# Kernel optimization log

Measured on AMD Instinct MI355X. Metric: run time of the kernel, lower is better.

The kernel has to match this reference:

```python
import jax, jax.numpy as jnp
import numpy as np

HIDDEN = 1024
FEAT = 2048
BOTTLENECK = 512
B, T = 64, 512


def setup_inputs() -> dict:
    key = jax.random.key(0)
    k1, k2, k3, k4, k5 = jax.random.split(key, 5)
    hidden = jax.random.normal(k1, (B, HIDDEN), dtype=jnp.float32)
    feats = jax.random.normal(k2, (B, T, FEAT), dtype=jnp.float32)
    # nn.Linear weights stored as [out, in]; apply as x @ W.T
    W = jax.random.normal(k3, (BOTTLENECK, HIDDEN), dtype=jnp.float32) * (1.0 / np.sqrt(HIDDEN))
    U = jax.random.normal(k4, (BOTTLENECK, FEAT), dtype=jnp.float32) * (1.0 / np.sqrt(FEAT))
    b = jnp.ones((BOTTLENECK,), dtype=jnp.float32)
    w = jax.random.normal(k5, (1, BOTTLENECK), dtype=jnp.float32) * (1.0 / np.sqrt(BOTTLENECK))
    return {"hidden": hidden, "feats": feats, "W": W, "U": U, "b": b, "w": w}


def reference(hidden, feats, W, U, b, w):
    Wh = hidden @ W.T                      # [B, K]
    Uv = jnp.einsum('btf,kf->btk', feats, U)  # [B, T, K]
    e = jnp.tanh(Wh[:, None, :] + Uv + b)  # [B, T, K]
    energies = jnp.einsum('btk,ok->bto', e, w)  # [B, T, 1]
    weights = jax.nn.softmax(energies, axis=1)  # softmax over time
    attn_feats = jnp.sum(feats * weights, axis=1)  # [B, F]
    return attn_feats, weights
```

## Files before the change

### kernel.cpp

```cpp
#include <hip/hip_runtime.h>
#include <math.h>

#define BATCH 64
#define TDIM 512
#define FEAT 2048
#define HID 1024
#define KDIM 512
#define MROWS (BATCH * TDIM)
#define TCH 16
#define TCLEN (TDIM / TCH)

#define NSTEP (FEAT / 64)
#define BSLOT (KDIM * 8)
#define BTILE (BSLOT * 8)

typedef __attribute__((ext_vector_type(8))) short short8;
typedef __attribute__((ext_vector_type(4))) float floatx4;

#define GLL16(g, l)                                                     \
    __builtin_amdgcn_global_load_lds(                                   \
        (const __attribute__((address_space(1))) void*)(g),             \
        (__attribute__((address_space(3))) void*)(l), 16, 0, 0)

__device__ __forceinline__ unsigned short f2bf(float x) {
    unsigned int u = __float_as_uint(x);
    u += 0x7FFFu + ((u >> 16) & 1u);
    return (unsigned short)(u >> 16);
}

__global__ __launch_bounds__(256) void k0n(const float* __restrict__ U,
                                           const float* __restrict__ hidden,
                                           const float* __restrict__ W,
                                           const float* __restrict__ bias,
                                           unsigned short* __restrict__ uBt,
                                           float* __restrict__ whb) {
    int bx = blockIdx.x;
    if (bx < 256) {
        const int NS = NSTEP * BSLOT;
        for (int s = bx * 256 + threadIdx.x; s < NS; s += 256 * 256) {
            int t   = s >> 12;
            int rem = s & 4095;
            int r   = rem >> 3;
            int c   = (rem & 7) ^ (r & 7);
            const float* src = U + (size_t)r * FEAT + t * 64 + c * 8;
            float4 v0 = *(const float4*)src;
            float4 v1 = *(const float4*)(src + 4);
            ushort4 o0, o1;
            o0.x = f2bf(v0.x); o0.y = f2bf(v0.y); o0.z = f2bf(v0.z); o0.w = f2bf(v0.w);
            o1.x = f2bf(v1.x); o1.y = f2bf(v1.y); o1.z = f2bf(v1.z); o1.w = f2bf(v1.w);
            ((ushort4*)uBt)[s * 2]     = o0;
            ((ushort4*)uBt)[s * 2 + 1] = o1;
        }
    } else {
        int bid = bx - 256;
        int b = bid >> 7;
        int k = (bid & 127) * 4 + (threadIdx.x >> 6);
        int lane = threadIdx.x & 63;
        const float* hrow = hidden + (size_t)b * HID;
        const float* wrow = W + (size_t)k * HID;
        float acc = 0.f;
        #pragma unroll 4
        for (int h = lane; h < HID; h += 64) acc += hrow[h] * wrow[h];
        #pragma unroll
        for (int off = 32; off > 0; off >>= 1) acc += __shfl_down(acc, off, 64);
        if (lane == 0) whb[b * KDIM + k] = acc + bias[k];
    }
}

__global__ __launch_bounds__(512, 2) void k2n(const float* __restrict__ feats,
                                              const unsigned short* __restrict__ uBt,
                                              const float* __restrict__ whb,
                                              const float* __restrict__ wvec,
                                              float* __restrict__ energies) {
    __shared__ __align__(16) unsigned short As[128 * 64];
    __shared__ __align__(16) unsigned short Bs[2][512 * 64];
    __shared__ float sums[4][128];

    const int tid  = threadIdx.x;
    const int wave = tid >> 6;
    const int lane = tid & 63;
    const int row0 = blockIdx.x * 128;
    const int wm = wave >> 2;
    const int wn = wave & 3;
    const int col = lane & 15, quad = lane >> 4;

    const int sr = tid >> 3;
    const int sc = (tid & 7) ^ (sr & 7);
    const float* gA = feats + (size_t)(row0 + sr) * FEAT + sc * 8;
    unsigned short* lA0 = As + tid * 8;
    unsigned short* lA1 = As + (tid + 512) * 8;

    const unsigned short* gB = uBt + (size_t)(wave * 512 + lane) * 8;

    floatx4 acc[4][8];
    #pragma unroll
    for (int i = 0; i < 4; ++i)
        #pragma unroll
        for (int j = 0; j < 8; ++j) acc[i][j] = (floatx4){0.f, 0.f, 0.f, 0.f};

    float4 a0 = *(const float4*)(gA);
    float4 a1 = *(const float4*)(gA + 4);
    float4 a2 = *(const float4*)(gA + (size_t)64 * FEAT);
    float4 a3 = *(const float4*)(gA + (size_t)64 * FEAT + 4);
    gA += 64;
    #pragma unroll
    for (int g = 0; g < 8; ++g)
        GLL16(gB + g * 512, &Bs[0][(wave * 512 + g * 64) * 8]);
    {
        short8 w0, w1;
        w0[0] = f2bf(a0.x); w0[1] = f2bf(a0.y); w0[2] = f2bf(a0.z); w0[3] = f2bf(a0.w);
        w0[4] = f2bf(a1.x); w0[5] = f2bf(a1.y); w0[6] = f2bf(a1.z); w0[7] = f2bf(a1.w);
        w1[0] = f2bf(a2.x); w1[1] = f2bf(a2.y); w1[2] = f2bf(a2.z); w1[3] = f2bf(a2.w);
        w1[4] = f2bf(a3.x); w1[5] = f2bf(a3.y); w1[6] = f2bf(a3.z); w1[7] = f2bf(a3.w);
        *(short8*)lA0 = w0;
        *(short8*)lA1 = w1;
    }
    __syncthreads();

    int nb = 0;
    for (int t = 0; t < NSTEP; ++t) {
        if (t < NSTEP - 1) {
            a0 = *(const float4*)(gA);
            a1 = *(const float4*)(gA + 4);
            a2 = *(const float4*)(gA + (size_t)64 * FEAT);
            a3 = *(const float4*)(gA + (size_t)64 * FEAT + 4);
            gA += 64;
            const unsigned short* gb = gB + (size_t)(t + 1) * BTILE;
            unsigned short* lb = &Bs[nb ^ 1][(wave * 512) * 8];
            #pragma unroll
            for (int g = 0; g < 8; ++g)
                GLL16(gb + g * 512, lb + g * 512);
        }

        #pragma unroll
        for (int kk = 0; kk < 2; ++kk) {
            const int sw = ((kk * 4 + quad) ^ (col & 7)) * 8;
            short8 af[4], bf[8];
            #pragma unroll
            for (int i = 0; i < 4; ++i)
                af[i] = *(const short8*)&As[(wm * 64 + i * 16 + col) * 64 + sw];
            #pragma unroll
            for (int j = 0; j < 8; ++j)
                bf[j] = *(const short8*)&Bs[nb][(wn * 128 + j * 16 + col) * 64 + sw];
            #pragma unroll
            for (int i = 0; i < 4; ++i)
                #pragma unroll
                for (int j = 0; j < 8; ++j)
                    acc[i][j] = __builtin_amdgcn_mfma_f32_16x16x32_bf16(
                        af[i], bf[j], acc[i][j], 0, 0, 0);
        }
        __syncthreads();

        if (t < NSTEP - 1) {
            short8 w0, w1;
            w0[0] = f2bf(a0.x); w0[1] = f2bf(a0.y); w0[2] = f2bf(a0.z); w0[3] = f2bf(a0.w);
            w0[4] = f2bf(a1.x); w0[5] = f2bf(a1.y); w0[6] = f2bf(a1.z); w0[7] = f2bf(a1.w);
            w1[0] = f2bf(a2.x); w1[1] = f2bf(a2.y); w1[2] = f2bf(a2.z); w1[3] = f2bf(a2.w);
            w1[4] = f2bf(a3.x); w1[5] = f2bf(a3.y); w1[6] = f2bf(a3.z); w1[7] = f2bf(a3.w);
            *(short8*)lA0 = w0;
            *(short8*)lA1 = w1;
            __syncthreads();
        }
        nb ^= 1;
    }

    const int b = row0 >> 9;
    float wk[8], hk[8];
    #pragma unroll
    for (int j = 0; j < 8; ++j) {
        int k = wn * 128 + j * 16 + col;
        wk[j] = wvec[k];
        hk[j] = whb[b * KDIM + k];
    }
    #pragma unroll
    for (int i = 0; i < 4; ++i) {
        #pragma unroll
        for (int r = 0; r < 4; ++r) {
            float s = 0.f;
            #pragma unroll
            for (int j = 0; j < 8; ++j)
                s += tanhf(acc[i][j][r] + hk[j]) * wk[j];
            #pragma unroll
            for (int off = 8; off > 0; off >>= 1)
                s += __shfl_down(s, off, 16);
            if (col == 0)
                sums[wn][wm * 64 + i * 16 + quad * 4 + r] = s;
        }
    }
    __syncthreads();
    if (tid < 128)
        energies[row0 + tid] =
            sums[0][tid] + sums[1][tid] + sums[2][tid] + sums[3][tid];
}

__global__ __launch_bounds__(512) void k3n(const float* __restrict__ energies,
                                           float* __restrict__ wout) {
    int b = blockIdx.x;
    int t = threadIdx.x;
    float e = energies[b * TDIM + t];

    __shared__ float sm[512];
    sm[t] = e;
    __syncthreads();
    #pragma unroll
    for (int s = 256; s > 0; s >>= 1) {
        if (t < s) sm[t] = fmaxf(sm[t], sm[t + s]);
        __syncthreads();
    }
    float m = sm[0];
    __syncthreads();
    float ex = __expf(e - m);
    sm[t] = ex;
    __syncthreads();
    #pragma unroll
    for (int s = 256; s > 0; s >>= 1) {
        if (t < s) sm[t] += sm[t + s];
        __syncthreads();
    }
    float inv = 1.f / sm[0];
    wout[b * TDIM + t] = ex * inv;
}

__global__ __launch_bounds__(256) void k4n(const float* __restrict__ feats,
                                           const float* __restrict__ weights,
                                           float* __restrict__ partial4) {
    int b  = blockIdx.y;
    int t0 = blockIdx.x * TCLEN;
    int f8 = threadIdx.x * 8;
    __shared__ float wsm[TCLEN];
    if (threadIdx.x < TCLEN) wsm[threadIdx.x] = weights[b * TDIM + t0 + threadIdx.x];
    __syncthreads();

    const float* fp = feats + ((size_t)b * TDIM + t0) * FEAT + f8;
    float a[8];
    #pragma unroll
    for (int e = 0; e < 8; ++e) a[e] = 0.f;
    #pragma unroll 4
    for (int t = 0; t < TCLEN; ++t) {
        float4 v0 = *(const float4*)(fp + (size_t)t * FEAT);
        float4 v1 = *(const float4*)(fp + (size_t)t * FEAT + 4);
        float w = wsm[t];
        a[0] += v0.x * w; a[1] += v0.y * w; a[2] += v0.z * w; a[3] += v0.w * w;
        a[4] += v1.x * w; a[5] += v1.y * w; a[6] += v1.z * w; a[7] += v1.w * w;
    }
    float* op = partial4 + ((size_t)blockIdx.x * BATCH + b) * FEAT + f8;
    float4 o0 = {a[0], a[1], a[2], a[3]};
    float4 o1 = {a[4], a[5], a[6], a[7]};
    *(float4*)op = o0;
    *(float4*)(op + 4) = o1;
}

__global__ __launch_bounds__(256) void k5_reduce(const float* __restrict__ partial4,
                                                 float* __restrict__ out) {
    int i4 = blockIdx.x * 256 + threadIdx.x;
    float4 s = ((const float4*)partial4)[i4];
    #pragma unroll
    for (int c = 1; c < TCH; ++c) {
        float4 v = ((const float4*)partial4)[(size_t)c * (BATCH * FEAT / 4) + i4];
        s.x += v.x; s.y += v.y; s.z += v.z; s.w += v.w;
    }
    ((float4*)out)[i4] = s;
}

#define BM 128
#define BN 128
#define BF 16
#define LDSPAD 4

__global__ __launch_bounds__(256) void k1_whb(const float* __restrict__ hidden,
                                              const float* __restrict__ W,
                                              const float* __restrict__ bias,
                                              float* __restrict__ whb) {
    int b = blockIdx.y;
    int k = blockIdx.x * 4 + (threadIdx.x >> 6);
    int lane = threadIdx.x & 63;
    const float* hrow = hidden + (size_t)b * HID;
    const float* wrow = W + (size_t)k * HID;
    float acc = 0.f;
    #pragma unroll 4
    for (int h = lane; h < HID; h += 64) acc += hrow[h] * wrow[h];
    #pragma unroll
    for (int off = 32; off > 0; off >>= 1) acc += __shfl_down(acc, off, 64);
    if (lane == 0) whb[b * KDIM + k] = acc + bias[k];
}

__global__ __launch_bounds__(256) void k2_energy(const float* __restrict__ feats,
                                                 const float* __restrict__ U,
                                                 const float* __restrict__ whb,
                                                 const float* __restrict__ wvec,
                                                 float* __restrict__ partial) {
    __shared__ __align__(16) float As[BF][BM + LDSPAD];
    __shared__ __align__(16) float Us[BF][BN + LDSPAD];

    const int row0 = blockIdx.x * BM;
    const int k0   = blockIdx.y * BN;
    const int tid  = threadIdx.x;
    const int tx   = tid & 15;
    const int ty   = tid >> 4;

    float acc[8][8];
    #pragma unroll
    for (int i = 0; i < 8; ++i)
        #pragma unroll
        for (int j = 0; j < 8; ++j) acc[i][j] = 0.f;

    for (int f0 = 0; f0 < FEAT; f0 += BF) {
        #pragma unroll
        for (int l = 0; l < 2; ++l) {
            int li = tid + l * 256;
            int r  = li >> 2;
            int c4 = (li & 3) * 4;
            float4 av = *(const float4*)(feats + (size_t)(row0 + r) * FEAT + f0 + c4);
            float4 uv = *(const float4*)(U     + (size_t)(k0   + r) * FEAT + f0 + c4);
            As[c4 + 0][r] = av.x; As[c4 + 1][r] = av.y;
            As[c4 + 2][r] = av.z; As[c4 + 3][r] = av.w;
            Us[c4 + 0][r] = uv.x; Us[c4 + 1][r] = uv.y;
            Us[c4 + 2][r] = uv.z; Us[c4 + 3][r] = uv.w;
        }
        __syncthreads();
        #pragma unroll
        for (int kf = 0; kf < BF; ++kf) {
            float4 a0 = *(const float4*)&As[kf][ty * 8];
            float4 a1 = *(const float4*)&As[kf][ty * 8 + 4];
            float4 u0 = *(const float4*)&Us[kf][tx * 8];
            float4 u1 = *(const float4*)&Us[kf][tx * 8 + 4];
            float a[8] = {a0.x, a0.y, a0.z, a0.w, a1.x, a1.y, a1.z, a1.w};
            float u[8] = {u0.x, u0.y, u0.z, u0.w, u1.x, u1.y, u1.z, u1.w};
            #pragma unroll
            for (int i = 0; i < 8; ++i)
                #pragma unroll
                for (int j = 0; j < 8; ++j) acc[i][j] += a[i] * u[j];
        }
        __syncthreads();
    }

    const int b = row0 >> 9;
    float psum[8];
    #pragma unroll
    for (int i = 0; i < 8; ++i) {
        float s = 0.f;
        #pragma unroll
        for (int j = 0; j < 8; ++j) {
            int k = k0 + tx * 8 + j;
            s += tanhf(acc[i][j] + whb[b * KDIM + k]) * wvec[k];
        }
        psum[i] = s;
    }
    #pragma unroll
    for (int off = 8; off > 0; off >>= 1)
        #pragma unroll
        for (int i = 0; i < 8; ++i) psum[i] += __shfl_down(psum[i], off, 16);

    if (tx == 0) {
        int c = blockIdx.y;
        #pragma unroll
        for (int i = 0; i < 8; ++i)
            partial[c * MROWS + row0 + ty * 8 + i] = psum[i];
    }
}

__global__ __launch_bounds__(512) void k3_softmax(const float* __restrict__ partial,
                                                  float* __restrict__ wout) {
    int b = blockIdx.x;
    int t = threadIdx.x;
    float e = 0.f;
    #pragma unroll
    for (int c = 0; c < 4; ++c) e += partial[c * MROWS + b * TDIM + t];

    __shared__ float sm[512];
    sm[t] = e;
    __syncthreads();
    #pragma unroll
    for (int s = 256; s > 0; s >>= 1) {
        if (t < s) sm[t] = fmaxf(sm[t], sm[t + s]);
        __syncthreads();
    }
    float m = sm[0];
    __syncthreads();
    float ex = __expf(e - m);
    sm[t] = ex;
    __syncthreads();
    #pragma unroll
    for (int s = 256; s > 0; s >>= 1) {
        if (t < s) sm[t] += sm[t + s];
        __syncthreads();
    }
    float inv = 1.f / sm[0];
    wout[b * TDIM + t] = ex * inv;
}

__global__ __launch_bounds__(256) void k4_direct(const float* __restrict__ feats,
                                                 const float* __restrict__ weights,
                                                 float* __restrict__ out) {
    int b = blockIdx.y;
    int f4 = (blockIdx.x * 256 + threadIdx.x) * 4;
    __shared__ float wsm[TDIM];
    wsm[threadIdx.x]       = weights[b * TDIM + threadIdx.x];
    wsm[threadIdx.x + 256] = weights[b * TDIM + 256 + threadIdx.x];
    __syncthreads();

    const float* fp = feats + (size_t)b * TDIM * FEAT + f4;
    float ax = 0.f, ay = 0.f, az = 0.f, aw = 0.f;
    for (int t = 0; t < TDIM; ++t) {
        float4 v = *(const float4*)(fp + (size_t)t * FEAT);
        float w = wsm[t];
        ax += v.x * w; ay += v.y * w; az += v.z * w; aw += v.w * w;
    }
    float4 o = {ax, ay, az, aw};
    *(float4*)(out + (size_t)b * FEAT + f4) = o;
}

extern "C" void kernel_launch(void* const* d_in, const int* in_sizes, int n_in,
                              void* d_out, int out_size, void* d_ws, size_t ws_size,
                              hipStream_t stream) {
    const float* hidden = (const float*)d_in[0];
    const float* feats  = (const float*)d_in[1];
    const float* W      = (const float*)d_in[2];
    const float* U      = (const float*)d_in[3];
    const float* bias   = (const float*)d_in[4];
    const float* wvec   = (const float*)d_in[5];

    float* out         = (float*)d_out;
    float* attn_out    = out;
    float* weights_out = out + (size_t)BATCH * FEAT;
    float* whb         = weights_out;
    float* energies    = attn_out;

    const size_t uN        = (size_t)KDIM * FEAT;
    const size_t uBytes    = uN * sizeof(unsigned short);
    const size_t poolBytes = (size_t)TCH * BATCH * FEAT * sizeof(float);
    const bool fast = ws_size >= uBytes + poolBytes;

    if (fast) {
        unsigned short* uBt = (unsigned short*)d_ws;
        float* pool4 = (float*)((char*)d_ws + uBytes);
        k0n<<<dim3(256 + 8192), 256, 0, stream>>>(U, hidden, W, bias, uBt, whb);
        k2n<<<dim3(MROWS / 128), 512, 0, stream>>>(feats, uBt, whb, wvec, energies);
        k3n<<<dim3(BATCH), 512, 0, stream>>>(energies, weights_out);
        k4n<<<dim3(TCH, BATCH), 256, 0, stream>>>(feats, weights_out, pool4);
        k5_reduce<<<dim3(BATCH * FEAT / 4 / 256), 256, 0, stream>>>(pool4, attn_out);
    } else {
        k1_whb<<<dim3(KDIM / 4, BATCH), 256, 0, stream>>>(hidden, W, bias, whb);
        k2_energy<<<dim3(MROWS / 128, KDIM / 128), 256, 0, stream>>>(
            feats, U, whb, wvec, energies);
        k3_softmax<<<dim3(BATCH), 512, 0, stream>>>(energies, weights_out);
        k4_direct<<<dim3(FEAT / 1024, BATCH), 256, 0, stream>>>(
            feats, weights_out, attn_out);
    }
}
```

Measured before the change: 499.6 us.

## Double-buffer A tile and use one barrier per K-step with manual vmcnt waits

Adds a second LDS buffer for the bf16-converted feats tile so the next A tile is converted and written while the current one is consumed. The two __syncthreads per iteration become a single s_barrier, with explicit s_waitcnt vmcnt/lgkmcnt and sched_barrier calls ordering the register A loads against the asynchronous B global_load_lds copies. B prefetch now runs two steps ahead into the buffer just freed. The reduction scratch reuses the A buffer, so LDS use rises to exactly 160KB. Correctness depends on the hand-counted vmcnt values matching the issue order.

```diff
diff --git a/kernel.cpp b/kernel.cpp
--- a/kernel.cpp
+++ b/kernel.cpp
@@ -21,6 +21,11 @@
     __builtin_amdgcn_global_load_lds(                                   \
         (const __attribute__((address_space(1))) void*)(g),             \
         (__attribute__((address_space(3))) void*)(l), 16, 0, 0)
+
+#define VMWAIT(N) asm volatile("s_waitcnt vmcnt(" #N ")" ::: "memory")
+#define LGKM0     asm volatile("s_waitcnt lgkmcnt(0)" ::: "memory")
+#define SCHEDB    __builtin_amdgcn_sched_barrier(0)
+#define SBAR      __builtin_amdgcn_s_barrier()
 
 __device__ __forceinline__ unsigned short f2bf(float x) {
     unsigned int u = __float_as_uint(x);
@@ -72,9 +77,8 @@
                                               const float* __restrict__ whb,
                                               const float* __restrict__ wvec,
                                               float* __restrict__ energies) {
-    __shared__ __align__(16) unsigned short As[128 * 64];
+    __shared__ __align__(16) unsigned short As[2][128 * 64];
     __shared__ __align__(16) unsigned short Bs[2][512 * 64];
-    __shared__ float sums[4][128];
 
     const int tid  = threadIdx.x;
     const int wave = tid >> 6;
@@ -87,8 +91,6 @@
     const int sr = tid >> 3;
     const int sc = (tid & 7) ^ (sr & 7);
     const float* gA = feats + (size_t)(row0 + sr) * FEAT + sc * 8;
-    unsigned short* lA0 = As + tid * 8;
-    unsigned short* lA1 = As + (tid + 512) * 8;
 
     const unsigned short* gB = uBt + (size_t)(wave * 512 + lane) * 8;
 
@@ -98,39 +100,52 @@
         #pragma unroll
         for (int j = 0; j < 8; ++j) acc[i][j] = (floatx4){0.f, 0.f, 0.f, 0.f};
 
-    float4 a0 = *(const float4*)(gA);
-    float4 a1 = *(const float4*)(gA + 4);
-    float4 a2 = *(const float4*)(gA + (size_t)64 * FEAT);
-    float4 a3 = *(const float4*)(gA + (size_t)64 * FEAT + 4);
-    gA += 64;
-    #pragma unroll
-    for (int g = 0; g < 8; ++g)
-        GLL16(gB + g * 512, &Bs[0][(wave * 512 + g * 64) * 8]);
-    {
-        short8 w0, w1;
-        w0[0] = f2bf(a0.x); w0[1] = f2bf(a0.y); w0[2] = f2bf(a0.z); w0[3] = f2bf(a0.w);
-        w0[4] = f2bf(a1.x); w0[5] = f2bf(a1.y); w0[6] = f2bf(a1.z); w0[7] = f2bf(a1.w);
-        w1[0] = f2bf(a2.x); w1[1] = f2bf(a2.y); w1[2] = f2bf(a2.z); w1[3] = f2bf(a2.w);
-        w1[4] = f2bf(a3.x); w1[5] = f2bf(a3.y); w1[6] = f2bf(a3.z); w1[7] = f2bf(a3.w);
-        *(short8*)lA0 = w0;
-        *(short8*)lA1 = w1;
-    }
-    __syncthreads();
-
-    int nb = 0;
+    float4 a0, a1, a2, a3;
+
+    #define LOAD_A()                                           \
+        do {                                                   \
+            a0 = *(const float4*)(gA);                         \
+            a1 = *(const float4*)(gA + 4);                     \
+            a2 = *(const float4*)(gA + (size_t)64 * FEAT);     \
+            a3 = *(const float4*)(gA + (size_t)64 * FEAT + 4); \
+            gA += 64;                                          \
+        } while (0)
+
+    #define CVT_WRITE_A(buf)                                                       \
+        do {                                                                       \
+            short8 w0, w1;                                                         \
+            w0[0] = f2bf(a0.x); w0[1] = f2bf(a0.y);                                \
+            w0[2] = f2bf(a0.z); w0[3] = f2bf(a0.w);                                \
+            w0[4] = f2bf(a1.x); w0[5] = f2bf(a1.y);                                \
+            w0[6] = f2bf(a1.z); w0[7] = f2bf(a1.w);                                \
+            w1[0] = f2bf(a2.x); w1[1] = f2bf(a2.y);                                \
+            w1[2] = f2bf(a2.z); w1[3] = f2bf(a2.w);                                \
+            w1[4] = f2bf(a3.x); w1[5] = f2bf(a3.y);                                \
+            w1[6] = f2bf(a3.z); w1[7] = f2bf(a3.w);                                \
+            *(short8*)&As[buf][tid * 8]         = w0;                              \
+            *(short8*)&As[buf][(tid + 512) * 8] = w1;                              \
+        } while (0)
+
+    #define ISSUE_B(tt, buf)                                               \
+        do {                                                               \
+            const unsigned short* gb = gB + (size_t)(tt) * BTILE;          \
+            unsigned short* lb = &Bs[buf][(wave * 512) * 8];               \
+            _Pragma("unroll")                                              \
+            for (int g = 0; g < 8; ++g) GLL16(gb + g * 512, lb + g * 512); \
+        } while (0)
+
+    LOAD_A();
+    ISSUE_B(0, 0);
+    VMWAIT(8); SCHEDB;
+    CVT_WRITE_A(0);
+    LOAD_A();
+    VMWAIT(4); SCHEDB;
+    LGKM0; SCHEDB;
+    SBAR; SCHEDB;
+    ISSUE_B(1, 1);
+
     for (int t = 0; t < NSTEP; ++t) {
-        if (t < NSTEP - 1) {
-            a0 = *(const float4*)(gA);
-            a1 = *(const float4*)(gA + 4);
-            a2 = *(const float4*)(gA + (size_t)64 * FEAT);
-            a3 = *(const float4*)(gA + (size_t)64 * FEAT + 4);
-            gA += 64;
-            const unsigned short* gb = gB + (size_t)(t + 1) * BTILE;
-            unsigned short* lb = &Bs[nb ^ 1][(wave * 512) * 8];
-            #pragma unroll
-            for (int g = 0; g < 8; ++g)
-                GLL16(gb + g * 512, lb + g * 512);
-        }
+        const int cur = t & 1, nxt = cur ^ 1;
 
         #pragma unroll
         for (int kk = 0; kk < 2; ++kk) {
@@ -138,10 +153,10 @@
             short8 af[4], bf[8];
             #pragma unroll
             for (int i = 0; i < 4; ++i)
-                af[i] = *(const short8*)&As[(wm * 64 + i * 16 + col) * 64 + sw];
+                af[i] = *(const short8*)&As[cur][(wm * 64 + i * 16 + col) * 64 + sw];
             #pragma unroll
             for (int j = 0; j < 8; ++j)
-                bf[j] = *(const short8*)&Bs[nb][(wn * 128 + j * 16 + col) * 64 + sw];
+                bf[j] = *(const short8*)&Bs[cur][(wn * 128 + j * 16 + col) * 64 + sw];
             #pragma unroll
             for (int i = 0; i < 4; ++i)
                 #pragma unroll
@@ -149,21 +164,26 @@
                     acc[i][j] = __builtin_amdgcn_mfma_f32_16x16x32_bf16(
                         af[i], bf[j], acc[i][j], 0, 0, 0);
         }
-        __syncthreads();
 
         if (t < NSTEP - 1) {
-            short8 w0, w1;
-            w0[0] = f2bf(a0.x); w0[1] = f2bf(a0.y); w0[2] = f2bf(a0.z); w0[3] = f2bf(a0.w);
-            w0[4] = f2bf(a1.x); w0[5] = f2bf(a1.y); w0[6] = f2bf(a1.z); w0[7] = f2bf(a1.w);
-            w1[0] = f2bf(a2.x); w1[1] = f2bf(a2.y); w1[2] = f2bf(a2.z); w1[3] = f2bf(a2.w);
-            w1[4] = f2bf(a3.x); w1[5] = f2bf(a3.y); w1[6] = f2bf(a3.z); w1[7] = f2bf(a3.w);
-            *(short8*)lA0 = w0;
-            *(short8*)lA1 = w1;
-            __syncthreads();
-        }
-        nb ^= 1;
-    }
-
+            VMWAIT(8); SCHEDB;
+            CVT_WRITE_A(nxt);
+            if (t < NSTEP - 2) {
+                LOAD_A();
+                VMWAIT(4); SCHEDB;
+            } else {
+                VMWAIT(0); SCHEDB;
+            }
+            LGKM0; SCHEDB;
+            SBAR; SCHEDB;
+            if (t < NSTEP - 2)
+                ISSUE_B(t + 2, cur);
+        }
+    }
+
+    __syncthreads();
+
+    float (*sums)[128] = (float (*)[128])As;
     const int b = row0 >> 9;
     float wk[8], hk[8];
     #pragma unroll
@@ -191,6 +211,10 @@
     if (tid < 128)
         energies[row0 + tid] =
             sums[0][tid] + sums[1][tid] + sums[2][tid] + sums[3][tid];
+
+    #undef LOAD_A
+    #undef CVT_WRITE_A
+    #undef ISSUE_B
 }
 
 __global__ __launch_bounds__(512) void k3n(const float* __restrict__ energies,
```

New measurement: 489.7 us. 1.02x faster.
